# Optimization experiments

Hardware: AMD Instinct MI355X
Metric: run time of the kernel (lower is better)

The kernel has to match this reference:

```python
import jax, jax.numpy as jnp
import numpy as np

T = 4096          # prefill tokens (single sequence)
HK = 16           # key heads
HV = 32           # value heads
DK = 128          # key head dim
DV = 128          # value head dim
K = 4             # causal conv kernel width
QKV = 2 * HK * DK + HV * DV  # 8192


def setup_inputs() -> dict:
    key = jax.random.key(0)
    k1, k2, k3, k4, k5, k6 = jax.random.split(key, 6)
    return {
        "mixed_qkv": jax.random.normal(k1, (T, QKV), dtype=jnp.float32),
        "a": jax.random.normal(k2, (T, HV), dtype=jnp.float32),
        "b": jax.random.normal(k3, (T, HV), dtype=jnp.float32),
        "conv_w": jax.random.normal(k4, (QKV, K), dtype=jnp.float32) * 0.2,
        "dt_bias": jax.random.normal(k5, (HV,), dtype=jnp.float32),
        "alog": jax.random.normal(k6, (HV,), dtype=jnp.float32),
    }


def _l2norm(x, eps=1e-6):
    return x * jax.lax.rsqrt(jnp.sum(x * x, axis=-1, keepdims=True) + eps)


def _forward(mixed_qkv, a, b, conv_w, dt_bias, alog):
    # --- causal depthwise conv1d (zero initial conv state) + SiLU ---
    xp = jnp.pad(mixed_qkv, ((K - 1, 0), (0, 0)))  # [T+K-1, QKV]
    y = sum(conv_w[None, :, j] * xp[j:j + T] for j in range(K))  # [T, QKV]
    x = jax.nn.silu(y)

    # --- split q/k/v ---
    q, k_, v = jnp.split(x, [HK * DK, 2 * HK * DK], axis=-1)
    q = q.reshape(T, HK, DK)
    k_ = k_.reshape(T, HK, DK)
    v = v.reshape(T, HV, DV)

    # use_qk_l2norm_in_kernel=True: L2-norm q,k; scale q by dk^-0.5
    q = _l2norm(q) * (DK ** -0.5)
    k_ = _l2norm(k_)

    # GQA: repeat key-head q/k to value-head count
    grp = HV // HK
    q = jnp.repeat(q, grp, axis=1)   # [T, HV, DK]
    k_ = jnp.repeat(k_, grp, axis=1)  # [T, HV, DK]

    # --- fused_gdn_gating ---
    g = -jnp.exp(alog)[None, :] * jax.nn.softplus(a + dt_bias[None, :])  # [T, HV]
    beta = jax.nn.sigmoid(b)                                             # [T, HV]

    # --- gated delta-rule recurrence (equiv. to chunk_gated_delta_rule) ---
    S0 = jnp.zeros((HV, DK, DV), dtype=mixed_qkv.dtype)

    def step(S, inp):
        qt, kt, vt, gt, bt = inp
        S = S * jnp.exp(gt)[:, None, None]                 # gated decay
        pred = jnp.einsum('hk,hkv->hv', kt, S)             # k^T S
        delta = (vt - pred) * bt[:, None]                  # beta-scaled error
        S = S + jnp.einsum('hk,hv->hkv', kt, delta)        # delta update
        o = jnp.einsum('hk,hkv->hv', qt, S)                # query readout
        return S, o

    _, out = jax.lax.scan(step, S0, (q, k_, v, g, beta))
    return out  # [T, HV, DV]


def reference(mixed_qkv, a, b, conv_w, dt_bias, alog):
    return _forward(mixed_qkv, a, b, conv_w, dt_bias, alog)
```

## Files before the change

### kernel.cpp

```cpp
#include <hip/hip_runtime.h>

#define T_LEN 4096
#define HKn   16
#define HVn   32
#define DKn   128
#define DVn   128
#define QKVn  8192
#define NCH   64
#define CS    64

typedef __attribute__((ext_vector_type(8))) short short8;
typedef __attribute__((ext_vector_type(4))) float f32x4;
typedef __attribute__((ext_vector_type(4))) unsigned u32x4;

#define OFF_QSH  ((size_t)0)
#define OFF_QSL  ((size_t)16777216)
#define OFF_KSH  ((size_t)33554432)
#define OFF_KSL  ((size_t)50331648)
#define OFF_KTH  ((size_t)67108864)
#define OFF_KTL  ((size_t)83886080)
#define OFF_VA   ((size_t)100663296)
#define OFF_GBL  ((size_t)167772160)
#define OFF_G    ((size_t)168820736)
#define OFF_WH   ((size_t)169345024)
#define OFF_WL   ((size_t)202899456)
#define OFF_MH   ((size_t)236453888)
#define OFF_ML   ((size_t)253231104)

template <int CTRL>
__device__ __forceinline__ float dpp_add(float x) {
    int v = __builtin_amdgcn_update_dpp(0, __float_as_int(x), CTRL, 0xF, 0xF, true);
    return x + __int_as_float(v);
}
__device__ __forceinline__ float reduce32g(float x) {
    x = dpp_add<0x128>(x); x = dpp_add<0x124>(x);
    x = dpp_add<0x122>(x); x = dpp_add<0x121>(x);
    int v = __builtin_amdgcn_ds_swizzle(__float_as_int(x), 0x401F);
    return x + __int_as_float(v);
}
__device__ __forceinline__ unsigned short bf16rne(float f) {
    unsigned x = __float_as_uint(f);
    return (unsigned short)((x + 0x7FFFu + ((x >> 16) & 1u)) >> 16);
}
__device__ __forceinline__ float bf16tof(unsigned short h) {
    return __uint_as_float(((unsigned)h) << 16);
}
__device__ __forceinline__ void bsplit(float f, unsigned short& h, unsigned short& l) {
    h = bf16rne(f);
    l = bf16rne(f - bf16tof(h));
}
__device__ __forceinline__ unsigned packsplit(float f) {
    unsigned short h, l; bsplit(f, h, l);
    return ((unsigned)h << 16) | (unsigned)l;
}
__device__ __forceinline__ f32x4 MF(short8 a, short8 b, f32x4 c) {
    return __builtin_amdgcn_mfma_f32_16x16x32_bf16(a, b, c, 0, 0, 0);
}
__device__ __forceinline__ void unpack8(u32x4 x0, u32x4 x1, short8& hi, short8& lo) {
    union { u32x4 u; short8 s; } H, L;
    H.u[0] = __builtin_amdgcn_perm(x0.y, x0.x, 0x07060302u);
    L.u[0] = __builtin_amdgcn_perm(x0.y, x0.x, 0x05040100u);
    H.u[1] = __builtin_amdgcn_perm(x0.w, x0.z, 0x07060302u);
    L.u[1] = __builtin_amdgcn_perm(x0.w, x0.z, 0x05040100u);
    H.u[2] = __builtin_amdgcn_perm(x1.y, x1.x, 0x07060302u);
    L.u[2] = __builtin_amdgcn_perm(x1.y, x1.x, 0x05040100u);
    H.u[3] = __builtin_amdgcn_perm(x1.w, x1.z, 0x07060302u);
    L.u[3] = __builtin_amdgcn_perm(x1.w, x1.z, 0x05040100u);
    hi = H.s; lo = L.s;
}
#define SB0() __builtin_amdgcn_sched_barrier(0)

__global__ __launch_bounds__(256) void k_gate(
    const float* __restrict__ a, const float* __restrict__ b,
    const float* __restrict__ dt_bias, const float* __restrict__ alog,
    float2* __restrict__ gbl)
{
    const int i = blockIdx.x * 256 + threadIdx.x;
    if (i < T_LEN * HVn) {
        const int h = i >> 12, t = i & (T_LEN - 1);
        const float av = a[(size_t)t * HVn + h];
        const float bv = b[(size_t)t * HVn + h];
        const float xv = av + dt_bias[h];
        const float sp = fmaxf(xv, 0.f) + log1pf(expf(-fabsf(xv)));
        const float g  = -expf(alog[h]) * sp;
        const float beta = 1.f / (1.f + expf(-bv));
        gbl[(size_t)h * T_LEN + t] = make_float2(beta, g);
    }
}

__global__ __launch_bounds__(128) void k_conv(
    const float* __restrict__ x, const float* __restrict__ w,
    const float* __restrict__ bgate,
    unsigned short* __restrict__ qsh, unsigned short* __restrict__ qsl,
    unsigned short* __restrict__ ksh, unsigned short* __restrict__ ksl,
    float* __restrict__ va2)
{
    const int t = blockIdx.x, seg = blockIdx.y, d = threadIdx.x;
    const int c = seg * 128 + d;
    const float4 w4 = ((const float4*)w)[c];
    float acc;
    if (t >= 3) {
        const float* xc = x + (size_t)(t - 3) * QKVn + c;
        acc = fmaf(w4.x, xc[0], fmaf(w4.y, xc[(size_t)QKVn],
              fmaf(w4.z, xc[(size_t)2 * QKVn], w4.w * xc[(size_t)3 * QKVn])));
    } else {
        float a0 = (t - 3 >= 0) ? x[(size_t)(t - 3) * QKVn + c] : 0.f;
        float a1 = (t - 2 >= 0) ? x[(size_t)(t - 2) * QKVn + c] : 0.f;
        float a2 = (t - 1 >= 0) ? x[(size_t)(t - 1) * QKVn + c] : 0.f;
        float a3 = x[(size_t)t * QKVn + c];
        acc = fmaf(w4.x, a0, fmaf(w4.y, a1, fmaf(w4.z, a2, w4.w * a3)));
    }
    const float y = acc / (1.f + expf(-acc));

    if (seg < 32) {
        float ss = reduce32g(y * y);
        __shared__ float part[4];
        if ((threadIdx.x & 31) == 0) part[threadIdx.x >> 5] = ss;
        __syncthreads();
        const float total = part[0] + part[1] + part[2] + part[3];
        const float r = rsqrtf(total + 1e-6f);
        float o = y * r;
        unsigned short hh, ll;
        if (seg < 16) {
            o *= 0.08838834764831845f;
            bsplit(o, hh, ll);
            const size_t idx = ((size_t)seg * T_LEN + t) * DKn + d;
            qsh[idx] = hh; qsl[idx] = ll;
        } else {
            bsplit(o, hh, ll);
            const size_t idx = ((size_t)(seg - 16) * T_LEN + t) * DKn + d;
            ksh[idx] = hh; ksl[idx] = ll;
        }
    } else {
        const int h = seg - 32;
        const float bv = bgate[(size_t)t * HVn + h];
        const float beta = 1.f / (1.f + expf(-bv));
        va2[((size_t)h * T_LEN + t) * DVn + d] = y * beta;
    }
}

__global__ __launch_bounds__(256) void k_tr(
    const unsigned short* __restrict__ ksh, const unsigned short* __restrict__ ksl,
    unsigned short* __restrict__ kth, unsigned short* __restrict__ ktl)
{
    __shared__ unsigned pk[64][65];
    const int b = blockIdx.x;
    const int kh = b >> 7, tt = (b >> 1) & 63, hh = b & 1;
    const int t0 = tt * 64, d0 = hh * 64;
    const int tid = threadIdx.x;
    #pragma unroll
    for (int e = 0; e < 16; ++e) {
        const int lin = e * 256 + tid;
        const int tl = lin >> 6, dl = lin & 63;
        const size_t o = ((size_t)kh * T_LEN + t0 + tl) * DKn + d0 + dl;
        pk[tl][dl] = ((unsigned)ksh[o] << 16) | (unsigned)ksl[o];
    }
    __syncthreads();
    #pragma unroll
    for (int e = 0; e < 16; ++e) {
        const int lin = e * 256 + tid;
        const int dl = lin >> 6, tl = lin & 63;
        const unsigned v = pk[tl][dl];
        const size_t o = ((size_t)kh * DKn + d0 + dl) * T_LEN + t0 + tl;
        kth[o] = (unsigned short)(v >> 16);
        ktl[o] = (unsigned short)(v & 0xFFFF);
    }
}

__global__ __launch_bounds__(256) void k_p1(
    const float2* __restrict__ gbl,
    const unsigned short* __restrict__ qsh, const unsigned short* __restrict__ qsl,
    const unsigned short* __restrict__ ksh, const unsigned short* __restrict__ ksl,
    float* __restrict__ va2, float* __restrict__ Gbuf,
    unsigned short* __restrict__ Wh, unsigned short* __restrict__ Wl,
    unsigned short* __restrict__ Mh, unsigned short* __restrict__ Ml)
{
    __shared__ float sA[64][68];
    __shared__ float sG[64];
    __shared__ float sB[64];
    const int blk = blockIdx.x;
    const int h = blk >> 6, ch = blk & 63;
    const int kh = h >> 1, t0 = ch * 64;
    const int tid = threadIdx.x, lane = tid & 63, wid = tid >> 6;
    const int l15 = lane & 15, lg = lane >> 4;

    if (tid < 64) {
        float2 g2 = gbl[(size_t)h * T_LEN + t0 + tid];
        sB[tid] = g2.x;
        float G = g2.y;
        #pragma unroll
        for (int s = 1; s < 64; s <<= 1) {
            float y = __int_as_float(__builtin_amdgcn_ds_bpermute((tid - s) << 2, __float_as_int(G)));
            G += (tid >= s) ? y : 0.f;
        }
        sG[tid] = G;
        Gbuf[(size_t)h * T_LEN + t0 + tid] = G;
    }
    __syncthreads();

    const char TIa[10] = {0,1,1,2,2,2,3,3,3,3};
    const char TJa[10] = {0,0,1,0,1,2,0,1,2,3};
    const size_t kbase = ((size_t)kh * T_LEN + t0) * DKn;
    for (int idx = wid; idx < 10; idx += 4) {
        const int mi = TIa[idx], nj = TJa[idx];
        f32x4 aKK = {0.f,0.f,0.f,0.f}, aQK = {0.f,0.f,0.f,0.f};
        #pragma unroll
        for (int kk = 0; kk < 4; ++kk) {
            const size_t offA = kbase + (size_t)(16*mi + l15) * DKn + 32*kk + 8*lg;
            const size_t offB = kbase + (size_t)(16*nj + l15) * DKn + 32*kk + 8*lg;
            short8 kAh = *(const short8*)(ksh + offA);
            short8 kAl = *(const short8*)(ksl + offA);
            short8 kBh = *(const short8*)(ksh + offB);
            short8 kBl = *(const short8*)(ksl + offB);
            short8 qAh = *(const short8*)(qsh + offA);
            short8 qAl = *(const short8*)(qsl + offA);
            aKK = MF(kAh,kBh,aKK); aKK = MF(kAh,kBl,aKK); aKK = MF(kAl,kBh,aKK);
            aQK = MF(qAh,kBh,aQK); aQK = MF(qAh,kBl,aQK); aQK = MF(qAl,kBh,aQK);
        }
        #pragma unroll
        for (int r = 0; r < 4; ++r) {
            const int i = 16*mi + 4*lg + r;
            const int j = 16*nj + l15;
            const float e = __expf(fminf(sG[i] - sG[j], 0.f));
            sA[i][j] = (j < i) ? sB[i] * e * aKK[r] : 0.f;
            const float mv = (j <= i) ? e * aQK[r] : 0.f;
            unsigned short mh, ml; bsplit(mv, mh, ml);
            const size_t moff = (((size_t)h * NCH + ch) * CS + i) * CS + j;
            Mh[moff] = mh; Ml[moff] = ml;
        }
    }
    __syncthreads();

    const int c = tid;
    float X[64];
    if (c < 128) {
        #pragma unroll
        for (int i = 0; i < 64; ++i)
            X[i] = va2[((size_t)h * T_LEN + t0 + i) * DVn + c];
    } else {
        const int dk = c - 128;
        #pragma unroll
        for (int i = 0; i < 64; ++i) {
            const size_t o = ((size_t)kh * T_LEN + t0 + i) * DKn + dk;
            const float kf = bf16tof(ksh[o]) + bf16tof(ksl[o]);
            X[i] = sB[i] * __expf(sG[i]) * kf;
        }
    }
    #pragma unroll
    for (int i = 1; i < 64; ++i) {
        float acc = X[i];
        const int nq = (i + 3) >> 2;
        #pragma unroll
        for (int q = 0; q < nq; ++q) {
            const f32x4 aa = *(const f32x4*)&sA[i][4*q];
            acc = fmaf(-aa[0], X[4*q+0], acc);
            acc = fmaf(-aa[1], X[4*q+1], acc);
            acc = fmaf(-aa[2], X[4*q+2], acc);
            acc = fmaf(-aa[3], X[4*q+3], acc);
        }
        X[i] = acc;
    }
    if (c < 128) {
        #pragma unroll
        for (int i = 0; i < 64; ++i)
            va2[((size_t)h * T_LEN + t0 + i) * DVn + c] = X[i];
    } else {
        const int dk = c - 128;
        #pragma unroll
        for (int i = 0; i < 64; ++i) {
            unsigned short wh, wl; bsplit(-X[i], wh, wl);
            const size_t o = (((size_t)h * NCH + ch) * CS + i) * DKn + dk;
            Wh[o] = wh; Wl[o] = wl;
        }
    }
}

struct ChBuf {
    short8 qh[4], ql[4];
    short8 wh[4], wl[4];
    short8 mh[2], ml[2];
    short8 th[2][2], tl[2][2];
    float  u[4];
    float4 g4;
    float  g63;
};

__device__ __forceinline__ void issue_ch(ChBuf& B, int ch,
    const unsigned short* __restrict__ qsh, const unsigned short* __restrict__ qsl,
    const unsigned short* __restrict__ kth, const unsigned short* __restrict__ ktl,
    const unsigned short* __restrict__ Wh, const unsigned short* __restrict__ Wl,
    const unsigned short* __restrict__ Mh, const unsigned short* __restrict__ Ml,
    const float* __restrict__ va2, const float* __restrict__ Gbuf,
    int h, int kh, int n0, int wid, int l15, int lg)
{
    const int t0 = ch * CS;
    const size_t qbase = ((size_t)kh * T_LEN + t0 + 16*wid + l15) * DKn;
    #pragma unroll
    for (int kk = 0; kk < 4; ++kk) {
        B.qh[kk] = *(const short8*)(qsh + qbase + 32*kk + 8*lg);
        B.ql[kk] = *(const short8*)(qsl + qbase + 32*kk + 8*lg);
    }
    const size_t wbase = (((size_t)h * NCH + ch) * CS + 16*wid + l15) * DKn;
    #pragma unroll
    for (int kk = 0; kk < 4; ++kk) {
        B.wh[kk] = *(const short8*)(Wh + wbase + 32*kk + 8*lg);
        B.wl[kk] = *(const short8*)(Wl + wbase + 32*kk + 8*lg);
    }
    const size_t mbase = (((size_t)h * NCH + ch) * CS + 16*wid + l15) * CS;
    #pragma unroll
    for (int k2 = 0; k2 < 2; ++k2) {
        B.mh[k2] = *(const short8*)(Mh + mbase + 32*k2 + 8*lg);
        B.ml[k2] = *(const short8*)(Ml + mbase + 32*k2 + 8*lg);
    }
    #pragma unroll
    for (int m2 = 0; m2 < 2; ++m2) {
        const size_t kb2 = ((size_t)kh * DKn + 16*(wid + 4*m2) + l15) * T_LEN + t0;
        #pragma unroll
        for (int k2 = 0; k2 < 2; ++k2) {
            B.th[m2][k2] = *(const short8*)(kth + kb2 + 32*k2 + 8*lg);
            B.tl[m2][k2] = *(const short8*)(ktl + kb2 + 32*k2 + 8*lg);
        }
    }
    #pragma unroll
    for (int r = 0; r < 4; ++r)
        B.u[r] = va2[((size_t)h * T_LEN + t0 + 16*wid + 4*lg + r) * DVn + n0 + l15];
    const float* gp = Gbuf + (size_t)h * T_LEN + t0;
    B.g4  = *(const float4*)(gp + 16*wid + 4*lg);
    B.g63 = gp[63];
}

__device__ __forceinline__ void compute_ch(const ChBuf& B, int ch,
    unsigned (*sSp)[132], unsigned (*sDLp)[68], unsigned (*sDSp)[68],
    short8* Sbh, short8* Sbl, f32x4* Sc,
    float* __restrict__ out,
    int h, int n0, int wid, int l15, int lg)
{
    const int t0 = ch * CS;
    const float g63 = B.g63;
    const float gr[4] = {B.g4.x, B.g4.y, B.g4.z, B.g4.w};

    f32x4 dl;
    #pragma unroll
    for (int r = 0; r < 4; ++r) dl[r] = B.u[r];
    #pragma unroll
    for (int kk = 0; kk < 4; ++kk) {
        dl = MF(B.wh[kk], Sbh[kk], dl); dl = MF(B.wh[kk], Sbl[kk], dl); dl = MF(B.wl[kk], Sbh[kk], dl);
    }

    const int cc0 = 16*wid + 4*lg;
    u32x4 pdl, pds;
    #pragma unroll
    for (int r = 0; r < 4; ++r) {
        pdl[r] = packsplit(dl[r]);
        pds[r] = packsplit(dl[r] * __expf(g63 - gr[r]));
    }
    *(u32x4*)&sDLp[l15][cc0] = pdl;
    *(u32x4*)&sDSp[l15][cc0] = pds;
    __syncthreads();

    short8 dlh[2], dll[2], dsh[2], dsl[2];
    #pragma unroll
    for (int k2 = 0; k2 < 2; ++k2) {
        u32x4 x0 = *(const u32x4*)&sDLp[l15][32*k2 + 8*lg];
        u32x4 x1 = *(const u32x4*)&sDLp[l15][32*k2 + 8*lg + 4];
        unpack8(x0, x1, dlh[k2], dll[k2]);
        u32x4 y0 = *(const u32x4*)&sDSp[l15][32*k2 + 8*lg];
        u32x4 y1 = *(const u32x4*)&sDSp[l15][32*k2 + 8*lg + 4];
        unpack8(y0, y1, dsh[k2], dsl[k2]);
    }

    f32x4 aq = {0.f,0.f,0.f,0.f}, am = {0.f,0.f,0.f,0.f};
    #pragma unroll
    for (int kk = 0; kk < 4; ++kk) {
        aq = MF(B.qh[kk], Sbh[kk], aq); aq = MF(B.qh[kk], Sbl[kk], aq); aq = MF(B.ql[kk], Sbh[kk], aq);
    }
    #pragma unroll
    for (int k2 = 0; k2 < 2; ++k2) {
        am = MF(B.mh[k2], dlh[k2], am); am = MF(B.mh[k2], dll[k2], am); am = MF(B.ml[k2], dlh[k2], am);
    }
    #pragma unroll
    for (int r = 0; r < 4; ++r) {
        const int cc = cc0 + r;
        out[((size_t)(t0 + cc) * HVn + h) * DVn + n0 + l15] = fmaf(__expf(gr[r]), aq[r], am[r]);
    }

    const float lam = __expf(g63);
    #pragma unroll
    for (int m2 = 0; m2 < 2; ++m2) {
        f32x4 t4 = {0.f,0.f,0.f,0.f};
        #pragma unroll
        for (int k2 = 0; k2 < 2; ++k2) {
            t4 = MF(B.th[m2][k2], dsh[k2], t4); t4 = MF(B.th[m2][k2], dsl[k2], t4); t4 = MF(B.tl[m2][k2], dsh[k2], t4);
        }
        u32x4 ps;
        #pragma unroll
        for (int r = 0; r < 4; ++r) {
            Sc[m2][r] = fmaf(lam, Sc[m2][r], t4[r]);
            ps[r] = packsplit(Sc[m2][r]);
        }
        *(u32x4*)&sSp[l15][16*wid + 64*m2 + 4*lg] = ps;
    }
    __syncthreads();

    #pragma unroll
    for (int kk = 0; kk < 4; ++kk) {
        u32x4 z0 = *(const u32x4*)&sSp[l15][32*kk + 8*lg];
        u32x4 z1 = *(const u32x4*)&sSp[l15][32*kk + 8*lg + 4];
        unpack8(z0, z1, Sbh[kk], Sbl[kk]);
    }
}

__global__ __launch_bounds__(256, 1) void k_p2(
    const unsigned short* __restrict__ qsh, const unsigned short* __restrict__ qsl,
    const unsigned short* __restrict__ kth, const unsigned short* __restrict__ ktl,
    const unsigned short* __restrict__ Wh, const unsigned short* __restrict__ Wl,
    const unsigned short* __restrict__ Mh, const unsigned short* __restrict__ Ml,
    const float* __restrict__ va2, const float* __restrict__ Gbuf,
    float* __restrict__ out)
{
    __shared__ unsigned sSp[16][132];
    __shared__ unsigned sDLp[16][68];
    __shared__ unsigned sDSp[16][68];

    const int p = blockIdx.x;
    const int slot = p >> 3;
    const int h  = (p & 7) * 4 + (slot & 3);
    const int nb = slot >> 2;
    const int kh = h >> 1, n0 = nb * 16;
    const int tid = threadIdx.x, lane = tid & 63, wid = tid >> 6;
    const int l15 = lane & 15, lg = lane >> 4;

    short8 Sbh[4], Sbl[4];
    f32x4 Sc[2];
    const short8 z8 = {0,0,0,0,0,0,0,0};
    #pragma unroll
    for (int kk = 0; kk < 4; ++kk) { Sbh[kk] = z8; Sbl[kk] = z8; }
    Sc[0] = (f32x4){0.f,0.f,0.f,0.f};
    Sc[1] = (f32x4){0.f,0.f,0.f,0.f};

    ChBuf bufA, bufB;
    issue_ch(bufA, 0, qsh, qsl, kth, ktl, Wh, Wl, Mh, Ml, va2, Gbuf,
             h, kh, n0, wid, l15, lg);

    #pragma unroll 1
    for (int ch2 = 0; ch2 < NCH / 2; ++ch2) {
        const int ch = 2 * ch2;
        SB0();
        issue_ch(bufB, ch + 1, qsh, qsl, kth, ktl, Wh, Wl, Mh, Ml, va2, Gbuf,
                 h, kh, n0, wid, l15, lg);
        SB0();
        compute_ch(bufA, ch, sSp, sDLp, sDSp, Sbh, Sbl, Sc, out, h, n0, wid, l15, lg);
        SB0();
        if (ch + 2 < NCH)
            issue_ch(bufA, ch + 2, qsh, qsl, kth, ktl, Wh, Wl, Mh, Ml, va2, Gbuf,
                     h, kh, n0, wid, l15, lg);
        SB0();
        compute_ch(bufB, ch + 1, sSp, sDLp, sDSp, Sbh, Sbl, Sc, out, h, n0, wid, l15, lg);
    }
}

extern "C" void kernel_launch(void* const* d_in, const int* in_sizes, int n_in,
                              void* d_out, int out_size, void* d_ws, size_t ws_size,
                              hipStream_t stream) {
    const float* mixed_qkv = (const float*)d_in[0];
    const float* a         = (const float*)d_in[1];
    const float* b         = (const float*)d_in[2];
    const float* conv_w    = (const float*)d_in[3];
    const float* dt_bias   = (const float*)d_in[4];
    const float* alog      = (const float*)d_in[5];
    float* out = (float*)d_out;
    char* ws = (char*)d_ws;

    unsigned short* qsh = (unsigned short*)(ws + OFF_QSH);
    unsigned short* qsl = (unsigned short*)(ws + OFF_QSL);
    unsigned short* ksh = (unsigned short*)(ws + OFF_KSH);
    unsigned short* ksl = (unsigned short*)(ws + OFF_KSL);
    unsigned short* kth = (unsigned short*)(ws + OFF_KTH);
    unsigned short* ktl = (unsigned short*)(ws + OFF_KTL);
    float*  va2 = (float*)(ws + OFF_VA);
    float2* gbl = (float2*)(ws + OFF_GBL);
    float*  Gbf = (float*)(ws + OFF_G);
    unsigned short* Wh = (unsigned short*)(ws + OFF_WH);
    unsigned short* Wl = (unsigned short*)(ws + OFF_WL);
    unsigned short* Mh = (unsigned short*)(ws + OFF_MH);
    unsigned short* Ml = (unsigned short*)(ws + OFF_ML);

    k_gate<<<(T_LEN * HVn + 255) / 256, 256, 0, stream>>>(a, b, dt_bias, alog, gbl);

    dim3 cgrid(T_LEN, 64);
    k_conv<<<cgrid, 128, 0, stream>>>(mixed_qkv, conv_w, b, qsh, qsl, ksh, ksl, va2);

    k_tr<<<2048, 256, 0, stream>>>(ksh, ksl, kth, ktl);

    k_p1<<<HVn * NCH, 256, 0, stream>>>(gbl, qsh, qsl, ksh, ksl, va2, Gbf, Wh, Wl, Mh, Ml);

    k_p2<<<HVn * 8, 256, 0, stream>>>(qsh, qsl, kth, ktl, Wh, Wl, Mh, Ml, va2, Gbf, out);
}
```

Baseline: 531.0 us.

## Split p2 recurrence into 8-column slices and break MFMA accumulation chains

The sequential chunk-recurrence kernel now gives each block 8 value columns instead of 16, doubling the grid to 512 blocks and allowing two blocks per CU. The MFMA tiles are still 16 wide, so half the lanes compute duplicated columns that are masked on store. The three-term split-precision MFMA chains are also split into independent accumulators summed at the end, shortening dependency latency on the serial critical path. In exchange the redundant MFMA work and duplicated loads of q, k and W per head double overall, and the summation order changes slightly.

Result: slower. 1.479 ms (+178.5%).

```diff
diff --git a/kernel.cpp b/kernel.cpp
--- a/kernel.cpp
+++ b/kernel.cpp
@@ -323,7 +323,7 @@
     }
     #pragma unroll
     for (int r = 0; r < 4; ++r)
-        B.u[r] = va2[((size_t)h * T_LEN + t0 + 16*wid + 4*lg + r) * DVn + n0 + l15];
+        B.u[r] = va2[((size_t)h * T_LEN + t0 + 16*wid + 4*lg + r) * DVn + n0 + (l15 & 7)];
     const float* gp = Gbuf + (size_t)h * T_LEN + t0;
     B.g4  = *(const float4*)(gp + 16*wid + 4*lg);
     B.g63 = gp[63];
@@ -339,13 +339,18 @@
     const float g63 = B.g63;
     const float gr[4] = {B.g4.x, B.g4.y, B.g4.z, B.g4.w};
 
+    f32x4 d0, d1, d2;
+    #pragma unroll
+    for (int r = 0; r < 4; ++r) { d0[r] = B.u[r]; d1[r] = 0.f; d2[r] = 0.f; }
+    #pragma unroll
+    for (int kk = 0; kk < 4; ++kk) {
+        d0 = MF(B.wh[kk], Sbh[kk], d0);
+        d1 = MF(B.wh[kk], Sbl[kk], d1);
+        d2 = MF(B.wl[kk], Sbh[kk], d2);
+    }
     f32x4 dl;
     #pragma unroll
-    for (int r = 0; r < 4; ++r) dl[r] = B.u[r];
-    #pragma unroll
-    for (int kk = 0; kk < 4; ++kk) {
-        dl = MF(B.wh[kk], Sbh[kk], dl); dl = MF(B.wh[kk], Sbl[kk], dl); dl = MF(B.wl[kk], Sbh[kk], dl);
-    }
+    for (int r = 0; r < 4; ++r) dl[r] = d0[r] + d1[r] + d2[r];
 
     const int cc0 = 16*wid + 4*lg;
     u32x4 pdl, pds;
@@ -369,36 +374,50 @@
         unpack8(y0, y1, dsh[k2], dsl[k2]);
     }
 
-    f32x4 aq = {0.f,0.f,0.f,0.f}, am = {0.f,0.f,0.f,0.f};
+    f32x4 a0, a1, a2, m0, m1, m2;
+    #pragma unroll
+    for (int r = 0; r < 4; ++r) { a0[r]=0.f; a1[r]=0.f; a2[r]=0.f; m0[r]=0.f; m1[r]=0.f; m2[r]=0.f; }
     #pragma unroll
     for (int kk = 0; kk < 4; ++kk) {
-        aq = MF(B.qh[kk], Sbh[kk], aq); aq = MF(B.qh[kk], Sbl[kk], aq); aq = MF(B.ql[kk], Sbh[kk], aq);
+        a0 = MF(B.qh[kk], Sbh[kk], a0);
+        a1 = MF(B.qh[kk], Sbl[kk], a1);
+        a2 = MF(B.ql[kk], Sbh[kk], a2);
     }
     #pragma unroll
     for (int k2 = 0; k2 < 2; ++k2) {
-        am = MF(B.mh[k2], dlh[k2], am); am = MF(B.mh[k2], dll[k2], am); am = MF(B.ml[k2], dlh[k2], am);
-    }
-    #pragma unroll
-    for (int r = 0; r < 4; ++r) {
-        const int cc = cc0 + r;
-        out[((size_t)(t0 + cc) * HVn + h) * DVn + n0 + l15] = fmaf(__expf(gr[r]), aq[r], am[r]);
+        m0 = MF(B.mh[k2], dlh[k2], m0);
+        m1 = MF(B.mh[k2], dll[k2], m1);
+        m2 = MF(B.ml[k2], dlh[k2], m2);
+    }
+    if (l15 < 8) {
+        #pragma unroll
+        for (int r = 0; r < 4; ++r) {
+            const int cc = cc0 + r;
+            const float aq = a0[r] + a1[r] + a2[r];
+            const float am = m0[r] + m1[r] + m2[r];
+            out[((size_t)(t0 + cc) * HVn + h) * DVn + n0 + l15] = fmaf(__expf(gr[r]), aq, am);
+        }
     }
 
     const float lam = __expf(g63);
     #pragma unroll
-    for (int m2 = 0; m2 < 2; ++m2) {
-        f32x4 t4 = {0.f,0.f,0.f,0.f};
+    for (int m2i = 0; m2i < 2; ++m2i) {
+        f32x4 t0a, t1a, t2a;
+        #pragma unroll
+        for (int r = 0; r < 4; ++r) { t0a[r]=0.f; t1a[r]=0.f; t2a[r]=0.f; }
         #pragma unroll
         for (int k2 = 0; k2 < 2; ++k2) {
-            t4 = MF(B.th[m2][k2], dsh[k2], t4); t4 = MF(B.th[m2][k2], dsl[k2], t4); t4 = MF(B.tl[m2][k2], dsh[k2], t4);
+            t0a = MF(B.th[m2i][k2], dsh[k2], t0a);
+            t1a = MF(B.th[m2i][k2], dsl[k2], t1a);
+            t2a = MF(B.tl[m2i][k2], dsh[k2], t2a);
         }
         u32x4 ps;
         #pragma unroll
         for (int r = 0; r < 4; ++r) {
-            Sc[m2][r] = fmaf(lam, Sc[m2][r], t4[r]);
-            ps[r] = packsplit(Sc[m2][r]);
-        }
-        *(u32x4*)&sSp[l15][16*wid + 64*m2 + 4*lg] = ps;
+            Sc[m2i][r] = fmaf(lam, Sc[m2i][r], t0a[r] + t1a[r] + t2a[r]);
+            ps[r] = packsplit(Sc[m2i][r]);
+        }
+        *(u32x4*)&sSp[l15][16*wid + 64*m2i + 4*lg] = ps;
     }
     __syncthreads();
 
@@ -410,7 +429,7 @@
     }
 }
 
-__global__ __launch_bounds__(256, 1) void k_p2(
+__global__ __launch_bounds__(256, 2) void k_p2(
     const unsigned short* __restrict__ qsh, const unsigned short* __restrict__ qsl,
     const unsigned short* __restrict__ kth, const unsigned short* __restrict__ ktl,
     const unsigned short* __restrict__ Wh, const unsigned short* __restrict__ Wl,
@@ -423,10 +442,11 @@
     __shared__ unsigned sDSp[16][68];
 
     const int p = blockIdx.x;
+    const int xcd = p & 7;
     const int slot = p >> 3;
-    const int h  = (p & 7) * 4 + (slot & 3);
+    const int h  = xcd * 4 + (slot & 3);
     const int nb = slot >> 2;
-    const int kh = h >> 1, n0 = nb * 16;
+    const int kh = h >> 1, n0 = nb * 8;
     const int tid = threadIdx.x, lane = tid & 63, wid = tid >> 6;
     const int l15 = lane & 15, lg = lane >> 4;
 
@@ -494,5 +514,5 @@
 
     k_p1<<<HVn * NCH, 256, 0, stream>>>(gbl, qsh, qsl, ksh, ksl, va2, Gbf, Wh, Wl, Mh, Ml);
 
-    k_p2<<<HVn * 8, 256, 0, stream>>>(qsh, qsl, kth, ktl, Wh, Wl, Mh, Ml, va2, Gbf, out);
-}
+    k_p2<<<HVn * 16, 256, 0, stream>>>(qsh, qsl, kth, ktl, Wh, Wl, Mh, Ml, va2, Gbf, out);
+}
```
